# Optimization experiments

Measured on AMD Instinct MI355X. Metric: run time of the kernel, lower is better.

The kernel has to match this reference:

```python
import jax, jax.numpy as jnp
import numpy as np

V = 100_000      # nodes
E = 300_000      # directed edges (no self loops)
IN = 256         # in_channels
OUT = 256        # out_channels
NREL2 = 474      # num_rel * 2
BN_EPS = 1e-5


def setup_inputs() -> dict:
    key = jax.random.key(0)
    ks = jax.random.split(key, 10)
    x = jax.random.normal(ks[0], (V, IN), dtype=jnp.float32)
    rel_repr = jax.random.normal(ks[1], (NREL2, IN), dtype=jnp.float32)
    # xavier_normal-ish init scale for params
    w = jax.random.normal(ks[2], (3, IN, OUT), dtype=jnp.float32) * (2.0 / (IN + OUT)) ** 0.5 * 1.414
    w_rel = jax.random.normal(ks[3], (IN, OUT), dtype=jnp.float32) * (2.0 / (IN + OUT)) ** 0.5 * 1.414
    loop_rel = jax.random.normal(ks[4], (1, IN), dtype=jnp.float32) * (2.0 / (1 + IN)) ** 0.5 * 1.414
    bias = jnp.zeros((OUT,), dtype=jnp.float32)
    src = jax.random.randint(ks[5], (E,), 0, V)
    dst = jax.random.randint(ks[6], (E,), 0, V)
    edge_type = jax.random.randint(ks[7], (E,), 0, NREL2)
    edge_dir = jax.random.randint(ks[8], (E,), 0, 2)
    return {"x": x, "rel_repr": rel_repr, "w": w, "w_rel": w_rel,
            "loop_rel": loop_rel, "bias": bias, "src": src, "dst": dst,
            "edge_type": edge_type, "edge_dir": edge_dir}


def reference(x, rel_repr, w, w_rel, loop_rel, bias, src, dst, edge_type, edge_dir):
    # edge norm: in_deg^-0.5(src) * in_deg^-0.5(dst), computed on graph w/o self loops
    deg = jax.ops.segment_sum(jnp.ones((E,), x.dtype), dst, num_segments=V)
    inv_sqrt = jnp.where(deg > 0, jax.lax.rsqrt(jnp.maximum(deg, 1.0)), 0.0)
    enorm = inv_sqrt[src] * inv_sqrt[dst]                      # [E]

    rel_all = jnp.concatenate([rel_repr, loop_rel], axis=0)    # [NREL2+1, IN]

    # compose (opn='mult'): h_src * rel[edge_type]
    ed = x[src] * rel_all[edge_type]                           # [E, IN]
    # direction-specific weight: bmm with w[dir], dir in {0,1} for real edges
    d0 = (edge_dir == 0)[:, None]
    msg = jnp.where(d0, ed, 0.0) @ w[0] + jnp.where(~d0, ed, 0.0) @ w[1]
    msg = msg * enorm[:, None]                                 # [E, OUT]
    agg = jax.ops.segment_sum(msg, dst, num_segments=V)        # scatter-sum

    # self-loops: type = NREL2 (loop_rel), dir = 2, norm = 1
    self_msg = (x * loop_rel) @ w[2]                           # [V, OUT]

    h = (agg + self_msg) / 3.0                                 # reduce_func: dropout(rate=0)/3
    h = h + bias

    # BatchNorm1d, training mode: batch stats, biased var, gamma=1, beta=0
    mean = jnp.mean(h, axis=0)
    var = jnp.var(h, axis=0)
    h = (h - mean) * jax.lax.rsqrt(var + BN_EPS)

    rel_out = (rel_all @ w_rel)[:, -1]                         # matches torch code's [:, -1]
    return h, rel_out
```

## Files before the change

### kernel.cpp

```cpp
#include <hip/hip_runtime.h>

#define V_N   100000
#define E_N   300000
#define IN_C  256
#define OUT_C 256
#define NREL2 474
#define BN_EPS 1e-5f
#define NB_SCAN 98
#define MTILES 391
#define BRCHUNK 98

typedef __attribute__((ext_vector_type(8))) short short8;
typedef __attribute__((ext_vector_type(4))) float f32x4;

__device__ __forceinline__ unsigned short f2bf(float f) {
    unsigned int u = __builtin_bit_cast(unsigned int, f);
    u += 0x7FFFu + ((u >> 16) & 1u);
    return (unsigned short)(u >> 16);
}
__device__ __forceinline__ unsigned int pk2bf(float lo, float hi) {
    return (unsigned int)f2bf(lo) | ((unsigned int)f2bf(hi) << 16);
}
__device__ __forceinline__ float blo(unsigned int u) {
    return __builtin_bit_cast(float, u << 16);
}
__device__ __forceinline__ float bhi(unsigned int u) {
    return __builtin_bit_cast(float, u & 0xFFFF0000u);
}

typedef const __attribute__((address_space(1))) unsigned int* gas1_t;
typedef __attribute__((address_space(3))) unsigned int* las3_t;
__device__ __forceinline__ void gload16(const void* g, void* l) {
    __builtin_amdgcn_global_load_lds((gas1_t)g, (las3_t)l, 16, 0, 0);
}


__global__ void count_kernel(const int* __restrict__ dst, int* __restrict__ cnt) {
    int e = blockIdx.x * 256 + threadIdx.x;
    if (e < E_N) atomicAdd(&cnt[dst[e]], 1);
}

__global__ __launch_bounds__(1024)
void scan1(const int* __restrict__ cnt, int* __restrict__ bsum, float* __restrict__ degi) {
    __shared__ int red[1024];
    int t = threadIdx.x;
    int v = blockIdx.x * 1024 + t;
    int c = (v < V_N) ? cnt[v] : 0;
    if (v < V_N) degi[v] = c > 0 ? rsqrtf((float)c) : 0.f;
    red[t] = c;
    __syncthreads();
    for (int s = 512; s > 0; s >>= 1) {
        if (t < s) red[t] += red[t + s];
        __syncthreads();
    }
    if (t == 0) bsum[blockIdx.x] = red[0];
}

__global__ void scan2(int* bsum) {
    __shared__ int sc[128];
    int t = threadIdx.x;
    int v = (t < NB_SCAN) ? bsum[t] : 0;
    sc[t] = v;
    __syncthreads();
    for (int d = 1; d < 128; d <<= 1) {
        int add = (t >= d) ? sc[t - d] : 0;
        __syncthreads();
        sc[t] += add;
        __syncthreads();
    }
    if (t < NB_SCAN) bsum[t] = sc[t] - v;
}

__global__ __launch_bounds__(1024)
void scan3(const int* __restrict__ cnt, const int* __restrict__ bsum,
           int* __restrict__ offs) {
    __shared__ int sc[1024];
    int t = threadIdx.x;
    int v = blockIdx.x * 1024 + t;
    int c = (v < V_N) ? cnt[v] : 0;
    sc[t] = c;
    __syncthreads();
    for (int d = 1; d < 1024; d <<= 1) {
        int add = (t >= d) ? sc[t - d] : 0;
        __syncthreads();
        sc[t] += add;
        __syncthreads();
    }
    if (v < V_N) offs[v] = sc[t] - c + bsum[blockIdx.x];
}

__global__ void scatter_kernel(const int* __restrict__ dst, const int* __restrict__ src,
                               const int* __restrict__ etype, const int* __restrict__ edir,
                               const int* __restrict__ offs, int* __restrict__ cursor,
                               int* __restrict__ epack) {
    int e = blockIdx.x * 256 + threadIdx.x;
    if (e < E_N) {
        int d = dst[e];
        int pos = offs[d] + atomicAdd(&cursor[d], 1);
        epack[pos] = src[e] | (etype[e] << 17) | (edir[e] << 26);
    }
}

__global__ void convert_w(const float* __restrict__ w, const float* __restrict__ loop_rel,
                          unsigned short* __restrict__ WcT) {
    int k = blockIdx.x;
    int n = threadIdx.x;
    float f = w[(size_t)k * 256 + n];
    if (k >= 512) f *= loop_rel[k - 512];
    WcT[(size_t)n * 768 + k] = f2bf(f);
}

__global__ void convert_x(const float* __restrict__ x, unsigned short* __restrict__ xbf) {
    const size_t total8 = (size_t)V_N * 32;
    size_t stride = (size_t)gridDim.x * blockDim.x;
    for (size_t idx = (size_t)blockIdx.x * blockDim.x + threadIdx.x; idx < total8; idx += stride) {
        const float* s = x + idx * 8;
        float4 a = *(const float4*)s, b = *(const float4*)(s + 4);
        uint4 u;
        u.x = pk2bf(a.x, a.y); u.y = pk2bf(a.z, a.w);
        u.z = pk2bf(b.x, b.y); u.w = pk2bf(b.z, b.w);
        *(uint4*)(xbf + idx * 8) = u;
    }
}

__global__ void convert_rel(const float* __restrict__ rel, unsigned short* __restrict__ relbf) {
    const int total8 = NREL2 * 32;
    int idx = blockIdx.x * 256 + threadIdx.x;
    if (idx < total8) {
        const float* s = rel + (size_t)idx * 8;
        float4 a = *(const float4*)s, b = *(const float4*)(s + 4);
        uint4 u;
        u.x = pk2bf(a.x, a.y); u.y = pk2bf(a.z, a.w);
        u.z = pk2bf(b.x, b.y); u.w = pk2bf(b.z, b.w);
        *(uint4*)(relbf + (size_t)idx * 8) = u;
    }
}

__global__ __launch_bounds__(256)
void aggregate(const unsigned short* __restrict__ xbf,
               const unsigned short* __restrict__ relbf,
               const float* __restrict__ degi,
               const int* __restrict__ cnt, const int* __restrict__ offs,
               const int* __restrict__ epack, unsigned short* __restrict__ Apre) {
    const int node = (blockIdx.x * 256 + threadIdx.x) >> 5;
    const int lane = threadIdx.x & 31;
    if (node >= V_N) return;
    const int v = node;
    const int n = cnt[v];
    const int base = offs[v];
    const float dv = degi[v];
    const int c8 = lane * 8;

    float a0[8] = {0,0,0,0,0,0,0,0};
    float a1[8] = {0,0,0,0,0,0,0,0};

    int i = 0;
    for (; i + 2 <= n; i += 2) {
        int p0 = epack[base + i];
        int p1 = epack[base + i + 1];
        int s0 = p0 & 0x1FFFF, s1 = p1 & 0x1FFFF;
        int t0 = (p0 >> 17) & 0x1FF, t1 = (p1 >> 17) & 0x1FF;
        float en0 = degi[s0] * dv, en1 = degi[s1] * dv;
        float e00 = (p0 & (1 << 26)) ? 0.f : en0, e01 = en0 - e00;
        float e10 = (p1 & (1 << 26)) ? 0.f : en1, e11 = en1 - e10;
        uint4 xu0 = *(const uint4*)(xbf   + (size_t)s0 * 256 + c8);
        uint4 ru0 = *(const uint4*)(relbf + (size_t)t0 * 256 + c8);
        uint4 xu1 = *(const uint4*)(xbf   + (size_t)s1 * 256 + c8);
        uint4 ru1 = *(const uint4*)(relbf + (size_t)t1 * 256 + c8);
        float m[8];
        m[0] = blo(xu0.x) * blo(ru0.x); m[1] = bhi(xu0.x) * bhi(ru0.x);
        m[2] = blo(xu0.y) * blo(ru0.y); m[3] = bhi(xu0.y) * bhi(ru0.y);
        m[4] = blo(xu0.z) * blo(ru0.z); m[5] = bhi(xu0.z) * bhi(ru0.z);
        m[6] = blo(xu0.w) * blo(ru0.w); m[7] = bhi(xu0.w) * bhi(ru0.w);
        #pragma unroll
        for (int j = 0; j < 8; j++) { a0[j] += m[j] * e00; a1[j] += m[j] * e01; }
        m[0] = blo(xu1.x) * blo(ru1.x); m[1] = bhi(xu1.x) * bhi(ru1.x);
        m[2] = blo(xu1.y) * blo(ru1.y); m[3] = bhi(xu1.y) * bhi(ru1.y);
        m[4] = blo(xu1.z) * blo(ru1.z); m[5] = bhi(xu1.z) * bhi(ru1.z);
        m[6] = blo(xu1.w) * blo(ru1.w); m[7] = bhi(xu1.w) * bhi(ru1.w);
        #pragma unroll
        for (int j = 0; j < 8; j++) { a0[j] += m[j] * e10; a1[j] += m[j] * e11; }
    }
    if (i < n) {
        int p = epack[base + i];
        int s = p & 0x1FFFF;
        int tt = (p >> 17) & 0x1FF;
        float en = degi[s] * dv;
        float e0 = (p & (1 << 26)) ? 0.f : en, e1 = en - e0;
        uint4 xu = *(const uint4*)(xbf   + (size_t)s * 256 + c8);
        uint4 ru = *(const uint4*)(relbf + (size_t)tt * 256 + c8);
        float m[8];
        m[0] = blo(xu.x) * blo(ru.x); m[1] = bhi(xu.x) * bhi(ru.x);
        m[2] = blo(xu.y) * blo(ru.y); m[3] = bhi(xu.y) * bhi(ru.y);
        m[4] = blo(xu.z) * blo(ru.z); m[5] = bhi(xu.z) * bhi(ru.z);
        m[6] = blo(xu.w) * blo(ru.w); m[7] = bhi(xu.w) * bhi(ru.w);
        #pragma unroll
        for (int j = 0; j < 8; j++) { a0[j] += m[j] * e0; a1[j] += m[j] * e1; }
    }

    uint4 u0, u1;
    u0.x = pk2bf(a0[0], a0[1]); u0.y = pk2bf(a0[2], a0[3]);
    u0.z = pk2bf(a0[4], a0[5]); u0.w = pk2bf(a0[6], a0[7]);
    u1.x = pk2bf(a1[0], a1[1]); u1.y = pk2bf(a1[2], a1[3]);
    u1.z = pk2bf(a1[4], a1[5]); u1.w = pk2bf(a1[6], a1[7]);
    *(uint4*)(Apre + (size_t)v * 512 + c8)       = u0;
    *(uint4*)(Apre + (size_t)v * 512 + 256 + c8) = u1;
}

__global__ __launch_bounds__(512)
void mfma_gemm(unsigned short* Ap ,
               const unsigned short* __restrict__ xbf,
               const unsigned short* __restrict__ WcT,
               const float* __restrict__ bias, float* __restrict__ partial) {
    __shared__ __align__(16) unsigned char smem[163840];

    const int t    = threadIdx.x;
    const int m0   = blockIdx.x * 256;
    const int wid  = t >> 6;
    const int lane = t & 63;
    const int wm   = wid >> 1;
    const int wn   = wid & 1;
    const int lr   = lane & 15;
    const int qk   = lane >> 4;
    const int sxr  = lr & 7;
    const int wbase = t & 0x1C0;

    int arow[4], acsw[4], brow[4], bcsw[4];
    #pragma unroll
    for (int j = 0; j < 4; ++j) {
        int g = j * 512 + t;
        arow[j] = g >> 3;
        acsw[j] = (g & 7) ^ (arow[j] & 7);
        brow[j] = g >> 3;
        bcsw[j] = (g & 7) ^ (brow[j] & 7);
    }

    auto A_lds = [&](int b3) { return (unsigned short*)(smem + b3 * 32768); };
    auto B_lds = [&](int b2) { return (unsigned short*)(smem + 98304 + b2 * 32768); };

    auto stageA = [&](int buf, int ks) {
        #pragma unroll
        for (int j = 0; j < 4; ++j) {
            int rg = m0 + arow[j];
            if (rg >= V_N) rg = V_N - 1;
            const unsigned short* s = (ks < 8)
                ? Ap  + (size_t)rg * 512 + ks * 64 + acsw[j] * 8
                : xbf + (size_t)rg * 256 + (ks - 8) * 64 + acsw[j] * 8;
            gload16(s, A_lds(buf) + (size_t)(j * 512 + wbase) * 8);
        }
    };
    auto stageB = [&](int buf, int ks) {
        #pragma unroll
        for (int j = 0; j < 4; ++j) {
            const unsigned short* s = WcT + (size_t)brow[j] * 768 + ks * 64 + bcsw[j] * 8;
            gload16(s, B_lds(buf) + (size_t)(j * 512 + wbase) * 8);
        }
    };

    f32x4 acc[4][8];
    #pragma unroll
    for (int m = 0; m < 4; m++)
        #pragma unroll
        for (int n = 0; n < 8; n++)
            acc[m][n] = (f32x4){0.f, 0.f, 0.f, 0.f};

    stageA(0, 0);
    stageB(0, 0);
    stageA(1, 1);

    #pragma unroll
    for (int ks = 0; ks < 12; ++ks) {
        const int a3 = ks % 3;
        const int b2 = ks & 1;
        if (ks < 11) { asm volatile("s_waitcnt vmcnt(4)" ::: "memory"); }
        else         { asm volatile("s_waitcnt vmcnt(0)" ::: "memory"); }
        __builtin_amdgcn_s_barrier();
        __builtin_amdgcn_sched_barrier(0);
        if (ks + 1 < 12) stageB((ks + 1) & 1, ks + 1);
        if (ks + 2 < 12) stageA((ks + 2) % 3, ks + 2);
        __builtin_amdgcn_sched_barrier(0);
        const unsigned short* Ab = A_lds(a3);
        const unsigned short* Bb = B_lds(b2);
        #pragma unroll
        for (int h = 0; h < 2; ++h) {
            short8 av[4], bv[8];
            #pragma unroll
            for (int m = 0; m < 4; m++)
                av[m] = *(const short8*)&Ab[(size_t)((wm * 64 + m * 16 + lr) * 8 + ((h * 4 + qk) ^ sxr)) * 8];
            #pragma unroll
            for (int n = 0; n < 8; n++)
                bv[n] = *(const short8*)&Bb[(size_t)((wn * 128 + n * 16 + lr) * 8 + ((h * 4 + qk) ^ sxr)) * 8];
            #pragma unroll
            for (int m = 0; m < 4; m++)
                #pragma unroll
                for (int n = 0; n < 8; n++)
                    acc[m][n] = __builtin_amdgcn_mfma_f32_16x16x32_bf16(av[m], bv[n], acc[m][n], 0, 0, 0);
        }
    }
    __syncthreads();

    unsigned short* Cst = (unsigned short*)smem;
    float* bs = (float*)(smem + 34816);
    bs[t] = 0.f;
    __syncthreads();

    const float inv3 = 1.f / 3.f;
    float bco[8];
    #pragma unroll
    for (int n = 0; n < 8; n++) bco[n] = bias[wn * 128 + n * 16 + lr];

    float s[8]  = {0.f, 0.f, 0.f, 0.f, 0.f, 0.f, 0.f, 0.f};
    float s2[8] = {0.f, 0.f, 0.f, 0.f, 0.f, 0.f, 0.f, 0.f};

    #pragma unroll
    for (int p = 0; p < 4; ++p) {
        if (wm == p) {
            #pragma unroll
            for (int m = 0; m < 4; m++) {
                #pragma unroll
                for (int n = 0; n < 8; n++) {
                    const int col = wn * 128 + n * 16 + lr;
                    #pragma unroll
                    for (int j = 0; j < 4; j++) {
                        int rl = m * 16 + qk * 4 + j;
                        float h = acc[m][n][j] * inv3 + bco[n];
                        if (m0 + p * 64 + rl < V_N) { s[n] += h; s2[n] += h * h; }
                        Cst[rl * 264 + col] = f2bf(h);
                    }
                }
            }
        }
        __syncthreads();
        #pragma unroll
        for (int i = 0; i < 4; ++i) {
            int f = t + i * 512;
            int row = f >> 5;
            int c8  = (f & 31) * 8;
            int r = m0 + p * 64 + row;
            if (r < V_N) {
                uint4 val = *(const uint4*)&Cst[row * 264 + c8];
                *(uint4*)&Ap[(size_t)r * 512 + c8] = val;
            }
        }
        __syncthreads();
    }

    #pragma unroll
    for (int n = 0; n < 8; n++) {
        s[n]  += __shfl_xor(s[n], 16);  s[n]  += __shfl_xor(s[n], 32);
        s2[n] += __shfl_xor(s2[n], 16); s2[n] += __shfl_xor(s2[n], 32);
    }
    if (lane < 16) {
        #pragma unroll
        for (int n = 0; n < 8; n++) {
            const int col = wn * 128 + n * 16 + lr;
            atomicAdd(&bs[col], s[n]);
            atomicAdd(&bs[256 + col], s2[n]);
        }
    }
    __syncthreads();
    partial[(size_t)blockIdx.x * 512 + t] = bs[t];
}


__global__ void bn_reduce_part(const float* __restrict__ partial, float* __restrict__ sums) {
    int t = threadIdx.x;
    int b0 = blockIdx.x * BRCHUNK;
    int b1 = b0 + BRCHUNK; if (b1 > MTILES) b1 = MTILES;
    float S = 0.f;
    for (int b = b0; b < b1; b++) S += partial[(size_t)b * 512 + t];
    atomicAdd(&sums[t], S);
}

__global__ void bn_finalize(const float* __restrict__ sums, float* __restrict__ ms) {
    int c = threadIdx.x;
    float mean = sums[c] / (float)V_N;
    float var  = sums[256 + c] / (float)V_N - mean * mean;
    ms[c]       = mean;
    ms[256 + c] = rsqrtf(var + BN_EPS);
}

__global__ void bn_norm2(const unsigned short* __restrict__ hbf,
                         const float* __restrict__ ms, float* __restrict__ out) {
    const size_t total8 = (size_t)V_N * 32;
    size_t stride = (size_t)gridDim.x * blockDim.x;
    for (size_t idx = (size_t)blockIdx.x * blockDim.x + threadIdx.x; idx < total8; idx += stride) {
        size_t v  = idx >> 5;
        int   c8  = (int)(idx & 31) * 8;
        uint4 uv = *(const uint4*)&hbf[v * 512 + c8];
        float4 ma = *(const float4*)&ms[c8];
        float4 mb = *(const float4*)&ms[c8 + 4];
        float4 ra = *(const float4*)&ms[256 + c8];
        float4 rb = *(const float4*)&ms[256 + c8 + 4];
        unsigned int w0 = uv.x, w1 = uv.y, w2 = uv.z, w3 = uv.w;
        float4 h0, h1;
        h0.x = (blo(w0) - ma.x) * ra.x;
        h0.y = (bhi(w0) - ma.y) * ra.y;
        h0.z = (blo(w1) - ma.z) * ra.z;
        h0.w = (bhi(w1) - ma.w) * ra.w;
        h1.x = (blo(w2) - mb.x) * rb.x;
        h1.y = (bhi(w2) - mb.y) * rb.y;
        h1.z = (blo(w3) - mb.z) * rb.z;
        h1.w = (bhi(w3) - mb.w) * rb.w;
        float* o = out + v * 256 + c8;
        *(float4*)o       = h0;
        *(float4*)(o + 4) = h1;
    }
}

__global__ void rel_out_kernel(const float* __restrict__ rel_repr,
                               const float* __restrict__ loop_rel,
                               const float* __restrict__ w_rel,
                               float* __restrict__ out)
{
    int r = blockIdx.x;
    const float* row = (r < NREL2) ? (rel_repr + (size_t)r * IN_C) : loop_rel;
    int l = threadIdx.x;
    float s = 0.f;
    #pragma unroll
    for (int q = 0; q < 4; q++) {
        int k = l + q * 64;
        s += row[k] * w_rel[(size_t)k * OUT_C + (OUT_C - 1)];
    }
    #pragma unroll
    for (int m = 32; m >= 1; m >>= 1) s += __shfl_xor(s, m);
    if (l == 0) out[(size_t)V_N * OUT_C + r] = s;
}


extern "C" void kernel_launch(void* const* d_in, const int* in_sizes, int n_in,
                              void* d_out, int out_size, void* d_ws, size_t ws_size,
                              hipStream_t stream) {
    const float* x        = (const float*)d_in[0];
    const float* rel_repr = (const float*)d_in[1];
    const float* w        = (const float*)d_in[2];
    const float* w_rel    = (const float*)d_in[3];
    const float* loop_rel = (const float*)d_in[4];
    const float* bias     = (const float*)d_in[5];
    const int*   src      = (const int*)d_in[6];
    const int*   dst      = (const int*)d_in[7];
    const int*   etype    = (const int*)d_in[8];
    const int*   edir     = (const int*)d_in[9];
    float* out = (float*)d_out;
    unsigned short* xbf = (unsigned short*)d_out;

    char* wsb = (char*)d_ws;
    int*   cnt     = (int*)(wsb + 0);
    int*   cursor  = (int*)(wsb + 400000);
    unsigned short* relbf = (unsigned short*)(wsb + 400000);
    int*   offs    = (int*)(wsb + 800000);
    float* degi    = (float*)(wsb + 1200000);
    int*   bsum    = (int*)(wsb + 1600000);
    float* partial = (float*)(wsb + 0);
    int*   epack   = (int*)(wsb + 1601792);
    float* ms      = (float*)(wsb + 2801792);
    float* sums    = (float*)(wsb + 2803840);
    unsigned short* WcT  = (unsigned short*)(wsb + 2805888);
    unsigned short* Apre = (unsigned short*)(wsb + 3199104);

    hipMemsetAsync(wsb, 0, 800000, stream);
    hipMemsetAsync(sums, 0, 2048, stream);

    count_kernel<<<(E_N + 255) / 256, 256, 0, stream>>>(dst, cnt);
    scan1<<<NB_SCAN, 1024, 0, stream>>>(cnt, bsum, degi);
    scan2<<<1, 128, 0, stream>>>(bsum);
    scan3<<<NB_SCAN, 1024, 0, stream>>>(cnt, bsum, offs);
    scatter_kernel<<<(E_N + 255) / 256, 256, 0, stream>>>(dst, src, etype, edir,
                                                          offs, cursor, epack);
    convert_w<<<768, 256, 0, stream>>>(w, loop_rel, WcT);
    convert_x<<<2048, 256, 0, stream>>>(x, xbf);
    convert_rel<<<(NREL2 * 32 + 255) / 256, 256, 0, stream>>>(rel_repr, relbf);
    aggregate<<<(V_N * 32 + 255) / 256, 256, 0, stream>>>(xbf, relbf, degi, cnt, offs,
                                                          epack, Apre);
    mfma_gemm<<<MTILES, 512, 0, stream>>>(Apre, xbf, WcT, bias, partial);
    bn_reduce_part<<<4, 512, 0, stream>>>(partial, sums);
    bn_finalize<<<1, 256, 0, stream>>>(sums, ms);
    bn_norm2<<<2048, 256, 0, stream>>>(Apre, ms, out);
    rel_out_kernel<<<NREL2 + 1, 64, 0, stream>>>(rel_repr, loop_rel, w_rel, out);
}
```

Before: 247.1 us.

## Merge small preprocessing kernels and fold BN finalize into normalization

Fuses the edge count with the x-to-bf16 conversion, merges scan1 with the weight and relation conversions, folds scan2 into scan3, and computes BN mean/rstd inside the normalize kernel from shared memory. This cuts the kernel launch count and lets independent small jobs run side by side instead of in sequence. The GEMM epilogue now stages 128 rows per pass instead of 64, using more shared memory and half as many barriers. relbf moves into the output buffer past xbf, which depends on that region not being overwritten before aggregate reads it.

```diff
diff --git a/kernel.cpp b/kernel.cpp
--- a/kernel.cpp
+++ b/kernel.cpp
@@ -9,6 +9,8 @@
 #define NB_SCAN 98
 #define MTILES 391
 #define BRCHUNK 98
+#define CNT_BLKS 1172
+#define CVX_BLKS 2048
 
 typedef __attribute__((ext_vector_type(8))) short short8;
 typedef __attribute__((ext_vector_type(4))) float f32x4;
@@ -35,47 +37,87 @@
 }
 
 
-__global__ void count_kernel(const int* __restrict__ dst, int* __restrict__ cnt) {
-    int e = blockIdx.x * 256 + threadIdx.x;
-    if (e < E_N) atomicAdd(&cnt[dst[e]], 1);
-}
+__global__ void count_convx(const int* __restrict__ dst, int* __restrict__ cnt,
+                            const float* __restrict__ x, unsigned short* __restrict__ xbf) {
+    if (blockIdx.x < CNT_BLKS) {
+        int e = blockIdx.x * 256 + threadIdx.x;
+        if (e < E_N) atomicAdd(&cnt[dst[e]], 1);
+    } else {
+        const size_t total8 = (size_t)V_N * 32;
+        const size_t stride = (size_t)CVX_BLKS * 256;
+        for (size_t idx = (size_t)(blockIdx.x - CNT_BLKS) * 256 + threadIdx.x;
+             idx < total8; idx += stride) {
+            const float* s = x + idx * 8;
+            float4 a = *(const float4*)s, b = *(const float4*)(s + 4);
+            uint4 u;
+            u.x = pk2bf(a.x, a.y); u.y = pk2bf(a.z, a.w);
+            u.z = pk2bf(b.x, b.y); u.w = pk2bf(b.z, b.w);
+            *(uint4*)(xbf + idx * 8) = u;
+        }
+    }
+}
+
 
 __global__ __launch_bounds__(1024)
-void scan1(const int* __restrict__ cnt, int* __restrict__ bsum, float* __restrict__ degi) {
-    __shared__ int red[1024];
+void scan1_conv(const int* __restrict__ cnt, int* __restrict__ bsum, float* __restrict__ degi,
+                const float* __restrict__ w, const float* __restrict__ loop_rel,
+                unsigned short* __restrict__ WcT,
+                const float* __restrict__ rel, unsigned short* __restrict__ relbf) {
+    const int bid = blockIdx.x;
+    const int t = threadIdx.x;
+    if (bid < NB_SCAN) {
+        __shared__ int red[1024];
+        int v = bid * 1024 + t;
+        int c = (v < V_N) ? cnt[v] : 0;
+        if (v < V_N) degi[v] = c > 0 ? rsqrtf((float)c) : 0.f;
+        red[t] = c;
+        __syncthreads();
+        for (int s = 512; s > 0; s >>= 1) {
+            if (t < s) red[t] += red[t + s];
+            __syncthreads();
+        }
+        if (t == 0) bsum[bid] = red[0];
+    } else if (bid < NB_SCAN + 192) {
+        int gid = (bid - NB_SCAN) * 1024 + t;
+        int k = gid >> 8;
+        int n = gid & 255;
+        float f = w[(size_t)k * 256 + n];
+        if (k >= 512) f *= loop_rel[k - 512];
+        WcT[(size_t)n * 768 + k] = f2bf(f);
+    } else {
+        int idx = (bid - NB_SCAN - 192) * 1024 + t;
+        if (idx < NREL2 * 32) {
+            const float* s = rel + (size_t)idx * 8;
+            float4 a = *(const float4*)s, b = *(const float4*)(s + 4);
+            uint4 u;
+            u.x = pk2bf(a.x, a.y); u.y = pk2bf(a.z, a.w);
+            u.z = pk2bf(b.x, b.y); u.w = pk2bf(b.z, b.w);
+            *(uint4*)(relbf + (size_t)idx * 8) = u;
+        }
+    }
+}
+
+
+__global__ __launch_bounds__(1024)
+void scan3b(const int* __restrict__ cnt, const int* __restrict__ bsum,
+            int* __restrict__ offs) {
+    __shared__ int sc[1024];
+    __shared__ int s2[128];
+    __shared__ int s2o[128];
+    __shared__ int sbase;
     int t = threadIdx.x;
-    int v = blockIdx.x * 1024 + t;
-    int c = (v < V_N) ? cnt[v] : 0;
-    if (v < V_N) degi[v] = c > 0 ? rsqrtf((float)c) : 0.f;
-    red[t] = c;
-    __syncthreads();
-    for (int s = 512; s > 0; s >>= 1) {
-        if (t < s) red[t] += red[t + s];
-        __syncthreads();
-    }
-    if (t == 0) bsum[blockIdx.x] = red[0];
-}
-
-__global__ void scan2(int* bsum) {
-    __shared__ int sc[128];
-    int t = threadIdx.x;
-    int v = (t < NB_SCAN) ? bsum[t] : 0;
-    sc[t] = v;
+    if (t < 128) {
+        int v = (t < NB_SCAN) ? bsum[t] : 0;
+        s2[t] = v; s2o[t] = v;
+    }
     __syncthreads();
     for (int d = 1; d < 128; d <<= 1) {
-        int add = (t >= d) ? sc[t - d] : 0;
-        __syncthreads();
-        sc[t] += add;
-        __syncthreads();
-    }
-    if (t < NB_SCAN) bsum[t] = sc[t] - v;
-}
-
-__global__ __launch_bounds__(1024)
-void scan3(const int* __restrict__ cnt, const int* __restrict__ bsum,
-           int* __restrict__ offs) {
-    __shared__ int sc[1024];
-    int t = threadIdx.x;
+        int add = (t < 128 && t >= d) ? s2[t - d] : 0;
+        __syncthreads();
+        if (t < 128) s2[t] += add;
+        __syncthreads();
+    }
+    if (t == 0) sbase = s2[blockIdx.x] - s2o[blockIdx.x];
     int v = blockIdx.x * 1024 + t;
     int c = (v < V_N) ? cnt[v] : 0;
     sc[t] = c;
@@ -86,7 +128,7 @@
         sc[t] += add;
         __syncthreads();
     }
-    if (v < V_N) offs[v] = sc[t] - c + bsum[blockIdx.x];
+    if (v < V_N) offs[v] = sc[t] - c + sbase;
 }
 
 __global__ void scatter_kernel(const int* __restrict__ dst, const int* __restrict__ src,
@@ -98,41 +140,6 @@
         int d = dst[e];
         int pos = offs[d] + atomicAdd(&cursor[d], 1);
         epack[pos] = src[e] | (etype[e] << 17) | (edir[e] << 26);
-    }
-}
-
-__global__ void convert_w(const float* __restrict__ w, const float* __restrict__ loop_rel,
-                          unsigned short* __restrict__ WcT) {
-    int k = blockIdx.x;
-    int n = threadIdx.x;
-    float f = w[(size_t)k * 256 + n];
-    if (k >= 512) f *= loop_rel[k - 512];
-    WcT[(size_t)n * 768 + k] = f2bf(f);
-}
-
-__global__ void convert_x(const float* __restrict__ x, unsigned short* __restrict__ xbf) {
-    const size_t total8 = (size_t)V_N * 32;
-    size_t stride = (size_t)gridDim.x * blockDim.x;
-    for (size_t idx = (size_t)blockIdx.x * blockDim.x + threadIdx.x; idx < total8; idx += stride) {
-        const float* s = x + idx * 8;
-        float4 a = *(const float4*)s, b = *(const float4*)(s + 4);
-        uint4 u;
-        u.x = pk2bf(a.x, a.y); u.y = pk2bf(a.z, a.w);
-        u.z = pk2bf(b.x, b.y); u.w = pk2bf(b.z, b.w);
-        *(uint4*)(xbf + idx * 8) = u;
-    }
-}
-
-__global__ void convert_rel(const float* __restrict__ rel, unsigned short* __restrict__ relbf) {
-    const int total8 = NREL2 * 32;
-    int idx = blockIdx.x * 256 + threadIdx.x;
-    if (idx < total8) {
-        const float* s = rel + (size_t)idx * 8;
-        float4 a = *(const float4*)s, b = *(const float4*)(s + 4);
-        uint4 u;
-        u.x = pk2bf(a.x, a.y); u.y = pk2bf(a.z, a.w);
-        u.z = pk2bf(b.x, b.y); u.w = pk2bf(b.z, b.w);
-        *(uint4*)(relbf + (size_t)idx * 8) = u;
     }
 }
 
@@ -300,7 +307,7 @@
     __syncthreads();
 
     unsigned short* Cst = (unsigned short*)smem;
-    float* bs = (float*)(smem + 34816);
+    float* bs = (float*)(smem + 67584);
     bs[t] = 0.f;
     __syncthreads();
 
@@ -313,8 +320,9 @@
     float s2[8] = {0.f, 0.f, 0.f, 0.f, 0.f, 0.f, 0.f, 0.f};
 
     #pragma unroll
-    for (int p = 0; p < 4; ++p) {
-        if (wm == p) {
+    for (int p = 0; p < 2; ++p) {
+        if ((wm >> 1) == p) {
+            const int rbase = (wm & 1) * 64;
             #pragma unroll
             for (int m = 0; m < 4; m++) {
                 #pragma unroll
@@ -322,9 +330,9 @@
                     const int col = wn * 128 + n * 16 + lr;
                     #pragma unroll
                     for (int j = 0; j < 4; j++) {
-                        int rl = m * 16 + qk * 4 + j;
+                        int rl = rbase + m * 16 + qk * 4 + j;
                         float h = acc[m][n][j] * inv3 + bco[n];
-                        if (m0 + p * 64 + rl < V_N) { s[n] += h; s2[n] += h * h; }
+                        if (m0 + p * 128 + rl < V_N) { s[n] += h; s2[n] += h * h; }
                         Cst[rl * 264 + col] = f2bf(h);
                     }
                 }
@@ -332,11 +340,11 @@
         }
         __syncthreads();
         #pragma unroll
-        for (int i = 0; i < 4; ++i) {
+        for (int i = 0; i < 8; ++i) {
             int f = t + i * 512;
             int row = f >> 5;
             int c8  = (f & 31) * 8;
-            int r = m0 + p * 64 + row;
+            int r = m0 + p * 128 + row;
             if (r < V_N) {
                 uint4 val = *(const uint4*)&Cst[row * 264 + c8];
                 *(uint4*)&Ap[(size_t)r * 512 + c8] = val;
@@ -372,36 +380,34 @@
     atomicAdd(&sums[t], S);
 }
 
-__global__ void bn_finalize(const float* __restrict__ sums, float* __restrict__ ms) {
-    int c = threadIdx.x;
-    float mean = sums[c] / (float)V_N;
-    float var  = sums[256 + c] / (float)V_N - mean * mean;
-    ms[c]       = mean;
-    ms[256 + c] = rsqrtf(var + BN_EPS);
-}
-
-__global__ void bn_norm2(const unsigned short* __restrict__ hbf,
-                         const float* __restrict__ ms, float* __restrict__ out) {
+__global__ __launch_bounds__(256)
+void bn_norm2f(const unsigned short* __restrict__ hbf, const float* __restrict__ sums,
+               float* __restrict__ out) {
+    __shared__ float msm[256], msr[256];
+    int tt = threadIdx.x;
+    {
+        float mean = sums[tt] * (1.0f / V_N);
+        float var  = sums[256 + tt] * (1.0f / V_N) - mean * mean;
+        msm[tt] = mean;
+        msr[tt] = rsqrtf(var + BN_EPS);
+    }
+    __syncthreads();
     const size_t total8 = (size_t)V_N * 32;
     size_t stride = (size_t)gridDim.x * blockDim.x;
-    for (size_t idx = (size_t)blockIdx.x * blockDim.x + threadIdx.x; idx < total8; idx += stride) {
+    for (size_t idx = (size_t)blockIdx.x * blockDim.x + tt; idx < total8; idx += stride) {
         size_t v  = idx >> 5;
         int   c8  = (int)(idx & 31) * 8;
         uint4 uv = *(const uint4*)&hbf[v * 512 + c8];
-        float4 ma = *(const float4*)&ms[c8];
-        float4 mb = *(const float4*)&ms[c8 + 4];
-        float4 ra = *(const float4*)&ms[256 + c8];
-        float4 rb = *(const float4*)&ms[256 + c8 + 4];
         unsigned int w0 = uv.x, w1 = uv.y, w2 = uv.z, w3 = uv.w;
         float4 h0, h1;
-        h0.x = (blo(w0) - ma.x) * ra.x;
-        h0.y = (bhi(w0) - ma.y) * ra.y;
-        h0.z = (blo(w1) - ma.z) * ra.z;
-        h0.w = (bhi(w1) - ma.w) * ra.w;
-        h1.x = (blo(w2) - mb.x) * rb.x;
-        h1.y = (bhi(w2) - mb.y) * rb.y;
-        h1.z = (blo(w3) - mb.z) * rb.z;
-        h1.w = (bhi(w3) - mb.w) * rb.w;
+        h0.x = (blo(w0) - msm[c8 + 0]) * msr[c8 + 0];
+        h0.y = (bhi(w0) - msm[c8 + 1]) * msr[c8 + 1];
+        h0.z = (blo(w1) - msm[c8 + 2]) * msr[c8 + 2];
+        h0.w = (bhi(w1) - msm[c8 + 3]) * msr[c8 + 3];
+        h1.x = (blo(w2) - msm[c8 + 4]) * msr[c8 + 4];
+        h1.y = (bhi(w2) - msm[c8 + 5]) * msr[c8 + 5];
+        h1.z = (blo(w3) - msm[c8 + 6]) * msr[c8 + 6];
+        h1.w = (bhi(w3) - msm[c8 + 7]) * msr[c8 + 7];
         float* o = out + v * 256 + c8;
         *(float4*)o       = h0;
         *(float4*)(o + 4) = h1;
@@ -442,18 +448,17 @@
     const int*   etype    = (const int*)d_in[8];
     const int*   edir     = (const int*)d_in[9];
     float* out = (float*)d_out;
-    unsigned short* xbf = (unsigned short*)d_out;
+    unsigned short* xbf   = (unsigned short*)d_out;
+    unsigned short* relbf = (unsigned short*)((char*)d_out + 51200000);
 
     char* wsb = (char*)d_ws;
     int*   cnt     = (int*)(wsb + 0);
     int*   cursor  = (int*)(wsb + 400000);
-    unsigned short* relbf = (unsigned short*)(wsb + 400000);
     int*   offs    = (int*)(wsb + 800000);
     float* degi    = (float*)(wsb + 1200000);
     int*   bsum    = (int*)(wsb + 1600000);
     float* partial = (float*)(wsb + 0);
     int*   epack   = (int*)(wsb + 1601792);
-    float* ms      = (float*)(wsb + 2801792);
     float* sums    = (float*)(wsb + 2803840);
     unsigned short* WcT  = (unsigned short*)(wsb + 2805888);
     unsigned short* Apre = (unsigned short*)(wsb + 3199104);
@@ -461,20 +466,17 @@
     hipMemsetAsync(wsb, 0, 800000, stream);
     hipMemsetAsync(sums, 0, 2048, stream);
 
-    count_kernel<<<(E_N + 255) / 256, 256, 0, stream>>>(dst, cnt);
-    scan1<<<NB_SCAN, 1024, 0, stream>>>(cnt, bsum, degi);
-    scan2<<<1, 128, 0, stream>>>(bsum);
-    scan3<<<NB_SCAN, 1024, 0, stream>>>(cnt, bsum, offs);
-    scatter_kernel<<<(E_N + 255) / 256, 256, 0, stream>>>(dst, src, etype, edir,
-                                                          offs, cursor, epack);
-    convert_w<<<768, 256, 0, stream>>>(w, loop_rel, WcT);
-    convert_x<<<2048, 256, 0, stream>>>(x, xbf);
-    convert_rel<<<(NREL2 * 32 + 255) / 256, 256, 0, stream>>>(rel_repr, relbf);
+    count_convx<<<CNT_BLKS + CVX_BLKS, 256, 0, stream>>>(dst, cnt, x, xbf);
+    scan1_conv<<<NB_SCAN + 192 + 15, 1024, 0, stream>>>(cnt, bsum, degi,
+                                                        w, loop_rel, WcT,
+                                                        rel_repr, relbf);
+    scan3b<<<NB_SCAN, 1024, 0, stream>>>(cnt, bsum, offs);
+    scatter_kernel<<<CNT_BLKS, 256, 0, stream>>>(dst, src, etype, edir,
+                                                 offs, cursor, epack);
     aggregate<<<(V_N * 32 + 255) / 256, 256, 0, stream>>>(xbf, relbf, degi, cnt, offs,
                                                           epack, Apre);
     mfma_gemm<<<MTILES, 512, 0, stream>>>(Apre, xbf, WcT, bias, partial);
     bn_reduce_part<<<4, 512, 0, stream>>>(partial, sums);
-    bn_finalize<<<1, 256, 0, stream>>>(sums, ms);
-    bn_norm2<<<2048, 256, 0, stream>>>(Apre, ms, out);
+    bn_norm2f<<<2048, 256, 0, stream>>>(Apre, sums, out);
     rel_out_kernel<<<NREL2 + 1, 64, 0, stream>>>(rel_repr, loop_rel, w_rel, out);
 }
```

New measurement: 228.3 us. -7.6%, faster.
